# Kernel optimization log

Measured on AMD Instinct MI355X. Metric: run time of the kernel, lower is better.

Reference implementation:

```python
import jax, jax.numpy as jnp
import numpy as np

B, N, F_IN, F_OUT, H = 8, 1024, 128, 128, 8
D_K = F_OUT // H
NEG = -1.0e9


def setup_inputs() -> dict:
    key = jax.random.key(0)
    ks = jax.random.split(key, 10)
    X = jax.random.normal(ks[0], (B, N, F_IN), dtype=jnp.float32)
    A = (jax.random.uniform(ks[1], (B, N, N)) < 0.1).astype(jnp.float32)
    A = jnp.maximum(A, jnp.eye(N, dtype=jnp.float32)[None])
    s_in = 1.0 / np.sqrt(F_IN)
    s_out = 1.0 / np.sqrt(F_OUT)
    Wq = jax.random.uniform(ks[2], (F_OUT, F_IN), minval=-s_in, maxval=s_in)
    bq = jax.random.uniform(ks[3], (F_OUT,), minval=-s_in, maxval=s_in)
    Wk = jax.random.uniform(ks[4], (F_OUT, F_IN), minval=-s_in, maxval=s_in)
    bk = jax.random.uniform(ks[5], (F_OUT,), minval=-s_in, maxval=s_in)
    Wv = jax.random.uniform(ks[6], (F_OUT, F_IN), minval=-s_in, maxval=s_in)
    bv = jax.random.uniform(ks[7], (F_OUT,), minval=-s_in, maxval=s_in)
    Wo = jax.random.uniform(ks[8], (F_OUT, F_OUT), minval=-s_out, maxval=s_out)
    bo = jax.random.uniform(ks[9], (F_OUT,), minval=-s_out, maxval=s_out)
    return {"X": X, "A": A, "Wq": Wq, "bq": bq, "Wk": Wk, "bk": bk,
            "Wv": Wv, "bv": bv, "Wo": Wo, "bo": bo}


def reference(X, A, Wq, bq, Wk, bk, Wv, bv, Wo, bo):
    # QKV projections (nn.Linear: x @ W.T + b), split into heads
    Q = (X @ Wq.T + bq).reshape(B, N, H, D_K).transpose(0, 2, 1, 3)  # [B,H,N,d]
    K = (X @ Wk.T + bk).reshape(B, N, H, D_K).transpose(0, 2, 1, 3)
    V = (X @ Wv.T + bv).reshape(B, N, H, D_K).transpose(0, 2, 1, 3)
    scores = jnp.einsum('bhnd,bhmd->bhnm', Q, K) / jnp.sqrt(
        jnp.asarray(D_K, dtype=Q.dtype))
    # adjacency mask: entries with A<=0 set to -1e9 (matches masked_fill)
    scores = jnp.where(A[:, None, :, :] > 0, scores, NEG)
    attn = jax.nn.softmax(scores, axis=-1)  # dropout is identity at eval
    out = jnp.einsum('bhnm,bhmd->bhnd', attn, V)
    out = out.transpose(0, 2, 1, 3).reshape(B, N, H * D_K)
    return out @ Wo.T + bo
```

## Files before the change

kernel.cpp:

```cpp
#include <hip/hip_runtime.h>
#include <hip/hip_bf16.h>


#define BATCH 8
#define NNODE 1024
#define FEAT  128
#define NHEAD 8
#define CHUNKW 96
#define SPADW  100

typedef __attribute__((ext_vector_type(8))) short short8v;
typedef __attribute__((ext_vector_type(4))) float float4v;

__device__ __forceinline__ unsigned short f2bf(float f) {
  union { float f; unsigned u; } c; c.f = f;
  unsigned u = c.u;
  u += 0x7fff + ((u >> 16) & 1);
  return (unsigned short)(u >> 16);
}
__device__ __forceinline__ float bf2f(unsigned short h) {
  union { unsigned u; float f; } c; c.u = ((unsigned)h) << 16;
  return c.f;
}


__global__ __launch_bounds__(256) void wconv_kernel(
    const float* __restrict__ Wq, const float* __restrict__ Wk,
    const float* __restrict__ Wv, const float* __restrict__ Wo,
    unsigned short* __restrict__ Wh, unsigned short* __restrict__ Wl) {
  const int m = blockIdx.x >> 3;
  const int p = blockIdx.x & 7;
  const float* src = (m == 0) ? Wq : (m == 1) ? Wk : (m == 2) ? Wv : Wo;
  const int c = p * 16 + (threadIdx.x >> 4);
  const int k0 = (threadIdx.x & 15) * 8;
  const float4 a = *(const float4*)&src[c * 128 + k0];
  const float4 b = *(const float4*)&src[c * 128 + k0 + 4];
  const float xs[8] = {a.x, a.y, a.z, a.w, b.x, b.y, b.z, b.w};
  short8v h8, l8;
  #pragma unroll
  for (int e = 0; e < 8; ++e) {
    const unsigned short hs = f2bf(xs[e]);
    h8[e] = (short)hs;
    l8[e] = (short)f2bf(xs[e] - bf2f(hs));
  }
  const int ks = k0 >> 5;
  const int kg = (k0 >> 3) & 3;
  const int lanep = (c & 15) + 16 * kg;
  const size_t off = ((((size_t)m * 8 + p) * 4 + ks) * 64 + lanep) * 8;
  *(short8v*)&Wh[off] = h8;
  *(short8v*)&Wl[off] = l8;
}

__global__ __launch_bounds__(256) void pack_x_kernel(
    const float* __restrict__ X,
    unsigned short* __restrict__ Xh, unsigned short* __restrict__ Xl) {
  const int rb = blockIdx.x;
  const int ks = threadIdx.x >> 6;
  const int lane = threadIdx.x & 63;
  const int r = rb * 16 + (lane & 15);
  const int k0 = ks * 32 + (lane >> 4) * 8;
  const float4 a = *(const float4*)&X[(size_t)r * 128 + k0];
  const float4 b = *(const float4*)&X[(size_t)r * 128 + k0 + 4];
  const float xs[8] = {a.x, a.y, a.z, a.w, b.x, b.y, b.z, b.w};
  short8v h8, l8;
  #pragma unroll
  for (int e = 0; e < 8; ++e) {
    const unsigned short hs = f2bf(xs[e]);
    h8[e] = (short)hs;
    l8[e] = (short)f2bf(xs[e] - bf2f(hs));
  }
  const size_t off = (((size_t)rb * 4 + ks) * 64 + lane) * 8;
  *(short8v*)&Xh[off] = h8;
  *(short8v*)&Xl[off] = l8;
}

__device__ __forceinline__ void mfma_body(
    const unsigned short* __restrict__ Wh, const unsigned short* __restrict__ Wl,
    int wtile0, const short8v* aH, const short8v* aL, float4v* acc) {
  const int l = threadIdx.x & 63;
  #pragma unroll
  for (int ks = 0; ks < 4; ++ks) {
    #pragma unroll
    for (int nt = 0; nt < 4; ++nt) {
      const size_t wb = ((((size_t)wtile0 + nt) * 4 + ks) * 64 + l) * 8;
      const short8v bh = *(const short8v*)&Wh[wb];
      const short8v bl = *(const short8v*)&Wl[wb];
      acc[nt] = __builtin_amdgcn_mfma_f32_16x16x32_bf16(aL[ks], bh, acc[nt], 0, 0, 0);
      acc[nt] = __builtin_amdgcn_mfma_f32_16x16x32_bf16(aH[ks], bl, acc[nt], 0, 0, 0);
      acc[nt] = __builtin_amdgcn_mfma_f32_16x16x32_bf16(aH[ks], bh, acc[nt], 0, 0, 0);
    }
  }
}

__global__ __launch_bounds__(256) void qkv_mfma_kernel(
    const unsigned short* __restrict__ Xh, const unsigned short* __restrict__ Xl,
    const unsigned short* __restrict__ Wh, const unsigned short* __restrict__ Wl,
    const float* __restrict__ bq, const float* __restrict__ bk,
    const float* __restrict__ bv,
    unsigned short* __restrict__ Q, unsigned short* __restrict__ K,
    unsigned short* __restrict__ V) {
  const int w = threadIdx.x >> 6;
  const int l = threadIdx.x & 63;
  const int rb = blockIdx.x * 4 + w;
  const int c0 = blockIdx.y * 64;
  const int m = blockIdx.z;
  const float* bias = (m == 0) ? bq : (m == 1) ? bk : bv;
  unsigned short* dst = (m == 0) ? Q : (m == 1) ? K : V;
  const float scale = (m == 0) ? 0.25f : 1.0f;

  short8v aH[4], aL[4];
  #pragma unroll
  for (int ks = 0; ks < 4; ++ks) {
    const size_t ab = (((size_t)rb * 4 + ks) * 64 + l) * 8;
    aH[ks] = *(const short8v*)&Xh[ab];
    aL[ks] = *(const short8v*)&Xl[ab];
  }
  float4v acc[4] = {};
  mfma_body(Wh, Wl, m * 8 + blockIdx.y * 4, aH, aL, acc);

  const int row16 = l & 15;
  const int kgrp = l >> 4;
  #pragma unroll
  for (int nt = 0; nt < 4; ++nt) {
    const int col = c0 + nt * 16 + row16;
    const float bcol = bias[col];
    #pragma unroll
    for (int r = 0; r < 4; ++r) {
      const int row = rb * 16 + kgrp * 4 + r;
      dst[(size_t)row * 128 + col] = f2bf((acc[nt][r] + bcol) * scale);
    }
  }
}

__global__ __launch_bounds__(256) void out_mfma_kernel(
    const unsigned short* __restrict__ Yh, const unsigned short* __restrict__ Yl,
    const unsigned short* __restrict__ Wh, const unsigned short* __restrict__ Wl,
    const float* __restrict__ bias, float* __restrict__ out) {
  const int w = threadIdx.x >> 6;
  const int l = threadIdx.x & 63;
  const int rb = blockIdx.x * 4 + w;
  const int c0 = blockIdx.y * 64;

  short8v aH[4], aL[4];
  #pragma unroll
  for (int ks = 0; ks < 4; ++ks) {
    const size_t ab = (((size_t)rb * 4 + ks) * 64 + l) * 8;
    aH[ks] = *(const short8v*)&Yh[ab];
    aL[ks] = *(const short8v*)&Yl[ab];
  }
  float4v acc[4] = {};
  mfma_body(Wh, Wl, 3 * 8 + blockIdx.y * 4, aH, aL, acc);

  const int row16 = l & 15;
  const int kgrp = l >> 4;
  #pragma unroll
  for (int nt = 0; nt < 4; ++nt) {
    const int col = c0 + nt * 16 + row16;
    const float bcol = bias[col];
    #pragma unroll
    for (int r = 0; r < 4; ++r) {
      const int row = rb * 16 + kgrp * 4 + r;
      out[(size_t)row * 128 + col] = acc[nt][r] + bcol;
    }
  }
}

__global__ __launch_bounds__(256) void attn_kernel(
    const unsigned short* __restrict__ Qb, const unsigned short* __restrict__ Kb,
    const unsigned short* __restrict__ Vb, const float* __restrict__ A,
    unsigned short* __restrict__ Yh, unsigned short* __restrict__ Yl) {
  __shared__ float sS[4][NHEAD][SPADW];
  __shared__ unsigned short sIdx[4][512];
  __shared__ float sAx[2][2][64];
  __shared__ float sAy[2][2][64];
  __shared__ float sLh[2][2][NHEAD];

  const int t = threadIdx.x;
  const int w = t >> 6;
  const int lane = t & 63;
  const int pw = w >> 1;
  const int half = w & 1;
  const int b = blockIdx.x & 7;
  const int i = ((blockIdx.x >> 3) << 1) + pw;
  const size_t bBase = (size_t)b * NNODE;
  const size_t rowQ = (bBase + i) * FEAT;

  float q0, q1, q2, q3;
  {
    const ushort4 qu = *(const ushort4*)&Qb[rowQ + 4 * (lane & 31)];
    q0 = bf2f(qu.x); q1 = bf2f(qu.y); q2 = bf2f(qu.z); q3 = bf2f(qu.w);
  }

  const float* Arow = A + (bBase + i) * NNODE + half * 512;
  const unsigned long long lt = (1ull << lane) - 1ull;
  int cnt = 0;
  #pragma unroll
  for (int r = 0; r < 2; ++r) {
    const float4 av = *(const float4*)&Arow[r * 256 + lane * 4];
    const unsigned long long m0 = __ballot(av.x > 0.f);
    const unsigned long long m1 = __ballot(av.y > 0.f);
    const unsigned long long m2 = __ballot(av.z > 0.f);
    const unsigned long long m3 = __ballot(av.w > 0.f);
    const int c0n = __popcll(m0), c1n = __popcll(m1), c2n = __popcll(m2);
    const int j0 = half * 512 + r * 256 + lane * 4;
    if (av.x > 0.f) sIdx[w][cnt + __popcll(m0 & lt)] = (unsigned short)j0;
    if (av.y > 0.f) sIdx[w][cnt + c0n + __popcll(m1 & lt)] = (unsigned short)(j0 + 1);
    if (av.z > 0.f) sIdx[w][cnt + c0n + c1n + __popcll(m2 & lt)] = (unsigned short)(j0 + 2);
    if (av.w > 0.f) sIdx[w][cnt + c0n + c1n + c2n + __popcll(m3 & lt)] = (unsigned short)(j0 + 3);
    cnt += c0n + c1n + c2n + __popcll(m3);
  }

  const int side = lane >> 5;
  const int sgrp = (lane & 31) >> 2;
  const int h = lane >> 3;
  float lacc = 0.f;
  float ax = 0.f, ay = 0.f;

  for (int c0 = 0; c0 < cnt; c0 += CHUNKW) {
    const int cs = min(cnt - c0, CHUNKW);

    for (int p2 = 0; p2 < cs; p2 += 2) {
      const int s = p2 + side;
      const bool valid = s < cs;
      const int j = sIdx[w][valid ? (c0 + s) : c0];
      const ushort4 ku = *(const ushort4*)&Kb[(bBase + j) * FEAT + 4 * (lane & 31)];
      float part = q0 * bf2f(ku.x) + q1 * bf2f(ku.y) +
                   q2 * bf2f(ku.z) + q3 * bf2f(ku.w);
      part += __shfl_xor(part, 1);
      part += __shfl_xor(part, 2);
      if (valid && (lane & 3) == 0) {
        const float p = __expf(part - 8.0f);
        sS[w][sgrp][s] = p;
        lacc += p;
      }
    }

    #pragma unroll 8
    for (int s = 0; s < cs; ++s) {
      const int j = sIdx[w][c0 + s];
      const unsigned vu = *(const unsigned*)&Vb[(bBase + j) * FEAT + 2 * lane];
      const float p = sS[w][h][s];
      ax += p * bf2f((unsigned short)(vu & 0xffff));
      ay += p * bf2f((unsigned short)(vu >> 16));
    }
  }

  const float lhv = __shfl(lacc, 4 * (lane & 7)) +
                    __shfl(lacc, 32 + 4 * (lane & 7));

  sAx[pw][half][lane] = ax;
  sAy[pw][half][lane] = ay;
  if (lane < NHEAD) sLh[pw][half][lane] = lhv;
  __syncthreads();

  const float axT = sAx[pw][0][lane] + sAx[pw][1][lane];
  const float ayT = sAy[pw][0][lane] + sAy[pw][1][lane];
  const float lT = sLh[pw][0][h] + sLh[pw][1][h];
  const float y0 = axT / lT;
  const float y1 = ayT / lT;

  const int grow = (int)(bBase + i);
  const int rb = grow >> 4;
  const int row16 = grow & 15;
  const int f0 = 2 * lane;
  const int ks = f0 >> 5;
  const int kg = (f0 >> 3) & 3;
  const int e0 = f0 & 7;
  const size_t off = (((size_t)rb * 4 + ks) * 64 + row16 + 16 * kg) * 8 + e0;
  const unsigned short h0 = f2bf(y0), h1 = f2bf(y1);
  if (half == 0) {
    *(unsigned*)&Yh[off] = (unsigned)h0 | ((unsigned)h1 << 16);
  } else {
    const unsigned short l0 = f2bf(y0 - bf2f(h0));
    const unsigned short l1 = f2bf(y1 - bf2f(h1));
    *(unsigned*)&Yl[off] = (unsigned)l0 | ((unsigned)l1 << 16);
  }
}

extern "C" void kernel_launch(void* const* d_in, const int* in_sizes, int n_in,
                              void* d_out, int out_size, void* d_ws, size_t ws_size,
                              hipStream_t stream) {
  const float* X  = (const float*)d_in[0];
  const float* A  = (const float*)d_in[1];
  const float* Wq = (const float*)d_in[2];
  const float* bq = (const float*)d_in[3];
  const float* Wk = (const float*)d_in[4];
  const float* bk = (const float*)d_in[5];
  const float* Wv = (const float*)d_in[6];
  const float* bv = (const float*)d_in[7];
  const float* Wo = (const float*)d_in[8];
  const float* bo = (const float*)d_in[9];
  float* out = (float*)d_out;

  const size_t mat = (size_t)BATCH * NNODE * FEAT;
  unsigned short* Q  = (unsigned short*)d_ws;
  unsigned short* K  = Q + mat;
  unsigned short* V  = K + mat;
  unsigned short* Yh = V + mat;
  unsigned short* Yl = Yh + mat;
  unsigned short* Xh = Yl + mat;
  unsigned short* Xl = Xh + mat;
  unsigned short* Wh = Xl + mat;
  unsigned short* Wl = Wh + 4 * 16384;

  hipLaunchKernelGGL(wconv_kernel, dim3(32), dim3(256), 0, stream,
                     Wq, Wk, Wv, Wo, Wh, Wl);
  hipLaunchKernelGGL(pack_x_kernel, dim3(512), dim3(256), 0, stream, X, Xh, Xl);
  hipLaunchKernelGGL(qkv_mfma_kernel, dim3(128, 2, 3), dim3(256), 0, stream,
                     Xh, Xl, Wh, Wl, bq, bk, bv, Q, K, V);
  hipLaunchKernelGGL(attn_kernel, dim3(4096), dim3(256), 0, stream,
                     Q, K, V, A, Yh, Yl);
  hipLaunchKernelGGL(out_mfma_kernel, dim3(128, 2), dim3(256), 0, stream,
                     Yh, Yl, Wh, Wl, bo, out);
}
```

Before: 146.8 us.

## Fuse all five stages into one cooperative persistent kernel with grid syncs

Replaces the five separate launches (weight conversion, X packing, QKV GEMM, attention, output GEMM) with a single cooperative kernel of 512 blocks. The blocks step through the stages and separate them with grid.sync(), looping over the attention tasks. The aim is to remove per-launch overhead and inter-kernel gaps. In exchange, occupancy is capped at 512 resident blocks, attention tasks are serialised in 8 iterations per block, and grid-wide barriers plus a cooperative-launch path add their own cost.

```diff
diff --git a/kernel.cpp b/kernel.cpp
--- a/kernel.cpp
+++ b/kernel.cpp
@@ -1,5 +1,8 @@
 #include <hip/hip_runtime.h>
 #include <hip/hip_bf16.h>
+#include <hip/hip_cooperative_groups.h>
+
+namespace cg = cooperative_groups;
 
 
 #define BATCH 8
@@ -24,12 +27,12 @@
 }
 
 
-__global__ __launch_bounds__(256) void wconv_kernel(
-    const float* __restrict__ Wq, const float* __restrict__ Wk,
+__device__ __forceinline__ void do_wconv(
+    int wb, const float* __restrict__ Wq, const float* __restrict__ Wk,
     const float* __restrict__ Wv, const float* __restrict__ Wo,
     unsigned short* __restrict__ Wh, unsigned short* __restrict__ Wl) {
-  const int m = blockIdx.x >> 3;
-  const int p = blockIdx.x & 7;
+  const int m = wb >> 3;
+  const int p = wb & 7;
   const float* src = (m == 0) ? Wq : (m == 1) ? Wk : (m == 2) ? Wv : Wo;
   const int c = p * 16 + (threadIdx.x >> 4);
   const int k0 = (threadIdx.x & 15) * 8;
@@ -51,10 +54,9 @@
   *(short8v*)&Wl[off] = l8;
 }
 
-__global__ __launch_bounds__(256) void pack_x_kernel(
-    const float* __restrict__ X,
+__device__ __forceinline__ void do_pack_x(
+    int rb, const float* __restrict__ X,
     unsigned short* __restrict__ Xh, unsigned short* __restrict__ Xl) {
-  const int rb = blockIdx.x;
   const int ks = threadIdx.x >> 6;
   const int lane = threadIdx.x & 63;
   const int r = rb * 16 + (lane & 15);
@@ -92,7 +94,8 @@
   }
 }
 
-__global__ __launch_bounds__(256) void qkv_mfma_kernel(
+__device__ __forceinline__ void do_qkv(
+    int tx, int ty, int tz,
     const unsigned short* __restrict__ Xh, const unsigned short* __restrict__ Xl,
     const unsigned short* __restrict__ Wh, const unsigned short* __restrict__ Wl,
     const float* __restrict__ bq, const float* __restrict__ bk,
@@ -101,12 +104,11 @@
     unsigned short* __restrict__ V) {
   const int w = threadIdx.x >> 6;
   const int l = threadIdx.x & 63;
-  const int rb = blockIdx.x * 4 + w;
-  const int c0 = blockIdx.y * 64;
-  const int m = blockIdx.z;
-  const float* bias = (m == 0) ? bq : (m == 1) ? bk : bv;
-  unsigned short* dst = (m == 0) ? Q : (m == 1) ? K : V;
-  const float scale = (m == 0) ? 0.25f : 1.0f;
+  const int rb = tx * 4 + w;
+  const int c0 = ty * 64;
+  const float* bias = (tz == 0) ? bq : (tz == 1) ? bk : bv;
+  unsigned short* dst = (tz == 0) ? Q : (tz == 1) ? K : V;
+  const float scale = (tz == 0) ? 0.25f : 1.0f;
 
   short8v aH[4], aL[4];
   #pragma unroll
@@ -116,7 +118,7 @@
     aL[ks] = *(const short8v*)&Xl[ab];
   }
   float4v acc[4] = {};
-  mfma_body(Wh, Wl, m * 8 + blockIdx.y * 4, aH, aL, acc);
+  mfma_body(Wh, Wl, tz * 8 + ty * 4, aH, aL, acc);
 
   const int row16 = l & 15;
   const int kgrp = l >> 4;
@@ -132,14 +134,15 @@
   }
 }
 
-__global__ __launch_bounds__(256) void out_mfma_kernel(
+__device__ __forceinline__ void do_out(
+    int tx, int ty,
     const unsigned short* __restrict__ Yh, const unsigned short* __restrict__ Yl,
     const unsigned short* __restrict__ Wh, const unsigned short* __restrict__ Wl,
     const float* __restrict__ bias, float* __restrict__ out) {
   const int w = threadIdx.x >> 6;
   const int l = threadIdx.x & 63;
-  const int rb = blockIdx.x * 4 + w;
-  const int c0 = blockIdx.y * 64;
+  const int rb = tx * 4 + w;
+  const int c0 = ty * 64;
 
   short8v aH[4], aL[4];
   #pragma unroll
@@ -149,7 +152,7 @@
     aL[ks] = *(const short8v*)&Yl[ab];
   }
   float4v acc[4] = {};
-  mfma_body(Wh, Wl, 3 * 8 + blockIdx.y * 4, aH, aL, acc);
+  mfma_body(Wh, Wl, 3 * 8 + ty * 4, aH, aL, acc);
 
   const int row16 = l & 15;
   const int kgrp = l >> 4;
@@ -165,7 +168,8 @@
   }
 }
 
-__global__ __launch_bounds__(256) void attn_kernel(
+__device__ __forceinline__ void do_attn(
+    int task,
     const unsigned short* __restrict__ Qb, const unsigned short* __restrict__ Kb,
     const unsigned short* __restrict__ Vb, const float* __restrict__ A,
     unsigned short* __restrict__ Yh, unsigned short* __restrict__ Yl) {
@@ -175,13 +179,15 @@
   __shared__ float sAy[2][2][64];
   __shared__ float sLh[2][2][NHEAD];
 
+  __syncthreads();
+
   const int t = threadIdx.x;
   const int w = t >> 6;
   const int lane = t & 63;
   const int pw = w >> 1;
   const int half = w & 1;
-  const int b = blockIdx.x & 7;
-  const int i = ((blockIdx.x >> 3) << 1) + pw;
+  const int b = task & 7;
+  const int i = ((task >> 3) << 1) + pw;
   const size_t bBase = (size_t)b * NNODE;
   const size_t rowQ = (bBase + i) * FEAT;
 
@@ -277,6 +283,41 @@
   }
 }
 
+__global__ __launch_bounds__(256, 2) void fused_kernel(
+    const float* __restrict__ X, const float* __restrict__ A,
+    const float* __restrict__ Wq, const float* __restrict__ bq,
+    const float* __restrict__ Wk, const float* __restrict__ bk,
+    const float* __restrict__ Wv, const float* __restrict__ bv,
+    const float* __restrict__ Wo, const float* __restrict__ bo,
+    float* __restrict__ out,
+    unsigned short* __restrict__ Qd, unsigned short* __restrict__ Kd,
+    unsigned short* __restrict__ Vd,
+    unsigned short* __restrict__ Yh, unsigned short* __restrict__ Yl,
+    unsigned short* __restrict__ Xh, unsigned short* __restrict__ Xl,
+    unsigned short* __restrict__ Wh, unsigned short* __restrict__ Wl) {
+  cg::grid_group grid = cg::this_grid();
+  const int bid = blockIdx.x;
+
+  do_pack_x(bid, X, Xh, Xl);
+  if (bid < 32) do_wconv(bid, Wq, Wk, Wv, Wo, Wh, Wl);
+  grid.sync();
+
+  do_qkv(bid & 127, (bid >> 7) & 1, bid >> 8, Xh, Xl, Wh, Wl,
+         bq, bk, bv, Qd, Kd, Vd);
+  if (bid < 256) {
+    const int t1 = bid + 512;
+    do_qkv(t1 & 127, (t1 >> 7) & 1, t1 >> 8, Xh, Xl, Wh, Wl,
+           bq, bk, bv, Qd, Kd, Vd);
+  }
+  grid.sync();
+
+  for (int it = 0; it < 8; ++it)
+    do_attn(bid + 512 * it, Qd, Kd, Vd, A, Yh, Yl);
+  grid.sync();
+
+  if (bid < 256) do_out(bid & 127, bid >> 7, Yh, Yl, Wh, Wl, bo, out);
+}
+
 extern "C" void kernel_launch(void* const* d_in, const int* in_sizes, int n_in,
                               void* d_out, int out_size, void* d_ws, size_t ws_size,
                               hipStream_t stream) {
@@ -293,23 +334,18 @@
   float* out = (float*)d_out;
 
   const size_t mat = (size_t)BATCH * NNODE * FEAT;
-  unsigned short* Q  = (unsigned short*)d_ws;
-  unsigned short* K  = Q + mat;
-  unsigned short* V  = K + mat;
-  unsigned short* Yh = V + mat;
+  unsigned short* Qd = (unsigned short*)d_ws;
+  unsigned short* Kd = Qd + mat;
+  unsigned short* Vd = Kd + mat;
+  unsigned short* Yh = Vd + mat;
   unsigned short* Yl = Yh + mat;
   unsigned short* Xh = Yl + mat;
   unsigned short* Xl = Xh + mat;
   unsigned short* Wh = Xl + mat;
   unsigned short* Wl = Wh + 4 * 16384;
 
-  hipLaunchKernelGGL(wconv_kernel, dim3(32), dim3(256), 0, stream,
-                     Wq, Wk, Wv, Wo, Wh, Wl);
-  hipLaunchKernelGGL(pack_x_kernel, dim3(512), dim3(256), 0, stream, X, Xh, Xl);
-  hipLaunchKernelGGL(qkv_mfma_kernel, dim3(128, 2, 3), dim3(256), 0, stream,
-                     Xh, Xl, Wh, Wl, bq, bk, bv, Q, K, V);
-  hipLaunchKernelGGL(attn_kernel, dim3(4096), dim3(256), 0, stream,
-                     Q, K, V, A, Yh, Yl);
-  hipLaunchKernelGGL(out_mfma_kernel, dim3(128, 2), dim3(256), 0, stream,
-                     Yh, Yl, Wh, Wl, bo, out);
-}
+  void* args[] = {&X, &A, &Wq, &bq, &Wk, &bk, &Wv, &bv, &Wo, &bo,
+                  &out, &Qd, &Kd, &Vd, &Yh, &Yl, &Xh, &Xl, &Wh, &Wl};
+  hipLaunchCooperativeKernel((const void*)fused_kernel, dim3(512), dim3(256),
+                             args, 0, stream);
+}
```

Result: slower. 405.0 us (+176.0%).

## Fuse output projection into attention kernel and merge prep kernels

Applied to the files above, without the earlier changes.

Merges the weight and X packing kernels into one launch and fuses the output projection into the attention kernel as an fp32 FMA loop reading Wo directly. This removes the Yh/Yl split-bf16 round trip and a separate MFMA launch. The QKV GEMM is also split into narrower column tiles to raise block count. In exchange, each attention block reads the full 64KB Wo from cache and does a scalar 2x128x128 GEMV per block, which adds ALU and L2 traffic to an already heavy kernel.

```diff
diff --git a/kernel.cpp b/kernel.cpp
--- a/kernel.cpp
+++ b/kernel.cpp
@@ -24,71 +24,55 @@
 }
 
 
-__global__ __launch_bounds__(256) void wconv_kernel(
+__global__ __launch_bounds__(256) void prep_kernel(
+    const float* __restrict__ X,
     const float* __restrict__ Wq, const float* __restrict__ Wk,
-    const float* __restrict__ Wv, const float* __restrict__ Wo,
+    const float* __restrict__ Wv,
+    unsigned short* __restrict__ Xh, unsigned short* __restrict__ Xl,
     unsigned short* __restrict__ Wh, unsigned short* __restrict__ Wl) {
-  const int m = blockIdx.x >> 3;
-  const int p = blockIdx.x & 7;
-  const float* src = (m == 0) ? Wq : (m == 1) ? Wk : (m == 2) ? Wv : Wo;
-  const int c = p * 16 + (threadIdx.x >> 4);
-  const int k0 = (threadIdx.x & 15) * 8;
-  const float4 a = *(const float4*)&src[c * 128 + k0];
-  const float4 b = *(const float4*)&src[c * 128 + k0 + 4];
-  const float xs[8] = {a.x, a.y, a.z, a.w, b.x, b.y, b.z, b.w};
-  short8v h8, l8;
-  #pragma unroll
-  for (int e = 0; e < 8; ++e) {
-    const unsigned short hs = f2bf(xs[e]);
-    h8[e] = (short)hs;
-    l8[e] = (short)f2bf(xs[e] - bf2f(hs));
-  }
-  const int ks = k0 >> 5;
-  const int kg = (k0 >> 3) & 3;
-  const int lanep = (c & 15) + 16 * kg;
-  const size_t off = ((((size_t)m * 8 + p) * 4 + ks) * 64 + lanep) * 8;
-  *(short8v*)&Wh[off] = h8;
-  *(short8v*)&Wl[off] = l8;
-}
-
-__global__ __launch_bounds__(256) void pack_x_kernel(
-    const float* __restrict__ X,
-    unsigned short* __restrict__ Xh, unsigned short* __restrict__ Xl) {
-  const int rb = blockIdx.x;
-  const int ks = threadIdx.x >> 6;
-  const int lane = threadIdx.x & 63;
-  const int r = rb * 16 + (lane & 15);
-  const int k0 = ks * 32 + (lane >> 4) * 8;
-  const float4 a = *(const float4*)&X[(size_t)r * 128 + k0];
-  const float4 b = *(const float4*)&X[(size_t)r * 128 + k0 + 4];
-  const float xs[8] = {a.x, a.y, a.z, a.w, b.x, b.y, b.z, b.w};
-  short8v h8, l8;
-  #pragma unroll
-  for (int e = 0; e < 8; ++e) {
-    const unsigned short hs = f2bf(xs[e]);
-    h8[e] = (short)hs;
-    l8[e] = (short)f2bf(xs[e] - bf2f(hs));
-  }
-  const size_t off = (((size_t)rb * 4 + ks) * 64 + lane) * 8;
-  *(short8v*)&Xh[off] = h8;
-  *(short8v*)&Xl[off] = l8;
-}
-
-__device__ __forceinline__ void mfma_body(
-    const unsigned short* __restrict__ Wh, const unsigned short* __restrict__ Wl,
-    int wtile0, const short8v* aH, const short8v* aL, float4v* acc) {
-  const int l = threadIdx.x & 63;
-  #pragma unroll
-  for (int ks = 0; ks < 4; ++ks) {
-    #pragma unroll
-    for (int nt = 0; nt < 4; ++nt) {
-      const size_t wb = ((((size_t)wtile0 + nt) * 4 + ks) * 64 + l) * 8;
-      const short8v bh = *(const short8v*)&Wh[wb];
-      const short8v bl = *(const short8v*)&Wl[wb];
-      acc[nt] = __builtin_amdgcn_mfma_f32_16x16x32_bf16(aL[ks], bh, acc[nt], 0, 0, 0);
-      acc[nt] = __builtin_amdgcn_mfma_f32_16x16x32_bf16(aH[ks], bl, acc[nt], 0, 0, 0);
-      acc[nt] = __builtin_amdgcn_mfma_f32_16x16x32_bf16(aH[ks], bh, acc[nt], 0, 0, 0);
-    }
+  const int bid = blockIdx.x;
+  if (bid < 512) {
+    const int rb = bid;
+    const int ks = threadIdx.x >> 6;
+    const int lane = threadIdx.x & 63;
+    const int r = rb * 16 + (lane & 15);
+    const int k0 = ks * 32 + (lane >> 4) * 8;
+    const float4 a = *(const float4*)&X[(size_t)r * 128 + k0];
+    const float4 b = *(const float4*)&X[(size_t)r * 128 + k0 + 4];
+    const float xs[8] = {a.x, a.y, a.z, a.w, b.x, b.y, b.z, b.w};
+    short8v h8, l8;
+    #pragma unroll
+    for (int e = 0; e < 8; ++e) {
+      const unsigned short hs = f2bf(xs[e]);
+      h8[e] = (short)hs;
+      l8[e] = (short)f2bf(xs[e] - bf2f(hs));
+    }
+    const size_t off = (((size_t)rb * 4 + ks) * 64 + lane) * 8;
+    *(short8v*)&Xh[off] = h8;
+    *(short8v*)&Xl[off] = l8;
+  } else {
+    const int wb = bid - 512;
+    const int m = wb >> 3;
+    const int p = wb & 7;
+    const float* src = (m == 0) ? Wq : (m == 1) ? Wk : Wv;
+    const int c = p * 16 + (threadIdx.x >> 4);
+    const int k0 = (threadIdx.x & 15) * 8;
+    const float4 a = *(const float4*)&src[c * 128 + k0];
+    const float4 b = *(const float4*)&src[c * 128 + k0 + 4];
+    const float xs[8] = {a.x, a.y, a.z, a.w, b.x, b.y, b.z, b.w};
+    short8v h8, l8;
+    #pragma unroll
+    for (int e = 0; e < 8; ++e) {
+      const unsigned short hs = f2bf(xs[e]);
+      h8[e] = (short)hs;
+      l8[e] = (short)f2bf(xs[e] - bf2f(hs));
+    }
+    const int ks = k0 >> 5;
+    const int kg = (k0 >> 3) & 3;
+    const int lanep = (c & 15) + 16 * kg;
+    const size_t off = ((((size_t)m * 8 + p) * 4 + ks) * 64 + lanep) * 8;
+    *(short8v*)&Wh[off] = h8;
+    *(short8v*)&Wl[off] = l8;
   }
 }
 
@@ -102,11 +86,12 @@
   const int w = threadIdx.x >> 6;
   const int l = threadIdx.x & 63;
   const int rb = blockIdx.x * 4 + w;
-  const int c0 = blockIdx.y * 64;
-  const int m = blockIdx.z;
-  const float* bias = (m == 0) ? bq : (m == 1) ? bk : bv;
-  unsigned short* dst = (m == 0) ? Q : (m == 1) ? K : V;
-  const float scale = (m == 0) ? 0.25f : 1.0f;
+  const int ty = blockIdx.y;
+  const int tz = blockIdx.z;
+  const int c0 = ty * 32;
+  const float* bias = (tz == 0) ? bq : (tz == 1) ? bk : bv;
+  unsigned short* dst = (tz == 0) ? Q : (tz == 1) ? K : V;
+  const float scale = (tz == 0) ? 0.25f : 1.0f;
 
   short8v aH[4], aL[4];
   #pragma unroll
@@ -115,13 +100,25 @@
     aH[ks] = *(const short8v*)&Xh[ab];
     aL[ks] = *(const short8v*)&Xl[ab];
   }
-  float4v acc[4] = {};
-  mfma_body(Wh, Wl, m * 8 + blockIdx.y * 4, aH, aL, acc);
+  float4v acc[2] = {};
+  const int wtile0 = tz * 8 + ty * 2;
+  #pragma unroll
+  for (int ks = 0; ks < 4; ++ks) {
+    #pragma unroll
+    for (int nt = 0; nt < 2; ++nt) {
+      const size_t wb = ((((size_t)wtile0 + nt) * 4 + ks) * 64 + l) * 8;
+      const short8v bh = *(const short8v*)&Wh[wb];
+      const short8v bl = *(const short8v*)&Wl[wb];
+      acc[nt] = __builtin_amdgcn_mfma_f32_16x16x32_bf16(aL[ks], bh, acc[nt], 0, 0, 0);
+      acc[nt] = __builtin_amdgcn_mfma_f32_16x16x32_bf16(aH[ks], bl, acc[nt], 0, 0, 0);
+      acc[nt] = __builtin_amdgcn_mfma_f32_16x16x32_bf16(aH[ks], bh, acc[nt], 0, 0, 0);
+    }
+  }
 
   const int row16 = l & 15;
   const int kgrp = l >> 4;
   #pragma unroll
-  for (int nt = 0; nt < 4; ++nt) {
+  for (int nt = 0; nt < 2; ++nt) {
     const int col = c0 + nt * 16 + row16;
     const float bcol = bias[col];
     #pragma unroll
@@ -132,48 +129,17 @@
   }
 }
 
-__global__ __launch_bounds__(256) void out_mfma_kernel(
-    const unsigned short* __restrict__ Yh, const unsigned short* __restrict__ Yl,
-    const unsigned short* __restrict__ Wh, const unsigned short* __restrict__ Wl,
-    const float* __restrict__ bias, float* __restrict__ out) {
-  const int w = threadIdx.x >> 6;
-  const int l = threadIdx.x & 63;
-  const int rb = blockIdx.x * 4 + w;
-  const int c0 = blockIdx.y * 64;
-
-  short8v aH[4], aL[4];
-  #pragma unroll
-  for (int ks = 0; ks < 4; ++ks) {
-    const size_t ab = (((size_t)rb * 4 + ks) * 64 + l) * 8;
-    aH[ks] = *(const short8v*)&Yh[ab];
-    aL[ks] = *(const short8v*)&Yl[ab];
-  }
-  float4v acc[4] = {};
-  mfma_body(Wh, Wl, 3 * 8 + blockIdx.y * 4, aH, aL, acc);
-
-  const int row16 = l & 15;
-  const int kgrp = l >> 4;
-  #pragma unroll
-  for (int nt = 0; nt < 4; ++nt) {
-    const int col = c0 + nt * 16 + row16;
-    const float bcol = bias[col];
-    #pragma unroll
-    for (int r = 0; r < 4; ++r) {
-      const int row = rb * 16 + kgrp * 4 + r;
-      out[(size_t)row * 128 + col] = acc[nt][r] + bcol;
-    }
-  }
-}
-
-__global__ __launch_bounds__(256) void attn_kernel(
+__global__ __launch_bounds__(256) void attn_out_kernel(
     const unsigned short* __restrict__ Qb, const unsigned short* __restrict__ Kb,
     const unsigned short* __restrict__ Vb, const float* __restrict__ A,
-    unsigned short* __restrict__ Yh, unsigned short* __restrict__ Yl) {
+    const float* __restrict__ Wo, const float* __restrict__ bo,
+    float* __restrict__ out) {
   __shared__ float sS[4][NHEAD][SPADW];
   __shared__ unsigned short sIdx[4][512];
   __shared__ float sAx[2][2][64];
   __shared__ float sAy[2][2][64];
   __shared__ float sLh[2][2][NHEAD];
+  __shared__ float sY[2][FEAT];
 
   const int t = threadIdx.x;
   const int w = t >> 6;
@@ -181,7 +147,8 @@
   const int pw = w >> 1;
   const int half = w & 1;
   const int b = blockIdx.x & 7;
-  const int i = ((blockIdx.x >> 3) << 1) + pw;
+  const int i0 = ((blockIdx.x >> 3) << 1);
+  const int i = i0 + pw;
   const size_t bBase = (size_t)b * NNODE;
   const size_t rowQ = (bBase + i) * FEAT;
 
@@ -253,28 +220,26 @@
   if (lane < NHEAD) sLh[pw][half][lane] = lhv;
   __syncthreads();
 
-  const float axT = sAx[pw][0][lane] + sAx[pw][1][lane];
-  const float ayT = sAy[pw][0][lane] + sAy[pw][1][lane];
-  const float lT = sLh[pw][0][h] + sLh[pw][1][h];
-  const float y0 = axT / lT;
-  const float y1 = ayT / lT;
-
-  const int grow = (int)(bBase + i);
-  const int rb = grow >> 4;
-  const int row16 = grow & 15;
-  const int f0 = 2 * lane;
-  const int ks = f0 >> 5;
-  const int kg = (f0 >> 3) & 3;
-  const int e0 = f0 & 7;
-  const size_t off = (((size_t)rb * 4 + ks) * 64 + row16 + 16 * kg) * 8 + e0;
-  const unsigned short h0 = f2bf(y0), h1 = f2bf(y1);
   if (half == 0) {
-    *(unsigned*)&Yh[off] = (unsigned)h0 | ((unsigned)h1 << 16);
-  } else {
-    const unsigned short l0 = f2bf(y0 - bf2f(h0));
-    const unsigned short l1 = f2bf(y1 - bf2f(h1));
-    *(unsigned*)&Yl[off] = (unsigned)l0 | ((unsigned)l1 << 16);
-  }
+    const float axT = sAx[pw][0][lane] + sAx[pw][1][lane];
+    const float ayT = sAy[pw][0][lane] + sAy[pw][1][lane];
+    const float lT = sLh[pw][0][h] + sLh[pw][1][h];
+    sY[pw][2 * lane] = axT / lT;
+    sY[pw][2 * lane + 1] = ayT / lT;
+  }
+  __syncthreads();
+
+  const int row = t >> 7;
+  const int c = t & 127;
+  const float* WoR = Wo + (size_t)c * FEAT;
+  const float* Yr = sY[row];
+  float acc = bo[c];
+  #pragma unroll 8
+  for (int k = 0; k < FEAT; k += 4) {
+    const float4 wv = *(const float4*)&WoR[k];
+    acc += Yr[k] * wv.x + Yr[k + 1] * wv.y + Yr[k + 2] * wv.z + Yr[k + 3] * wv.w;
+  }
+  out[(bBase + i0 + row) * FEAT + c] = acc;
 }
 
 extern "C" void kernel_launch(void* const* d_in, const int* in_sizes, int n_in,
@@ -293,23 +258,18 @@
   float* out = (float*)d_out;
 
   const size_t mat = (size_t)BATCH * NNODE * FEAT;
-  unsigned short* Q  = (unsigned short*)d_ws;
-  unsigned short* K  = Q + mat;
-  unsigned short* V  = K + mat;
-  unsigned short* Yh = V + mat;
-  unsigned short* Yl = Yh + mat;
-  unsigned short* Xh = Yl + mat;
+  unsigned short* Qd = (unsigned short*)d_ws;
+  unsigned short* Kd = Qd + mat;
+  unsigned short* Vd = Kd + mat;
+  unsigned short* Xh = Vd + mat;
   unsigned short* Xl = Xh + mat;
   unsigned short* Wh = Xl + mat;
-  unsigned short* Wl = Wh + 4 * 16384;
-
-  hipLaunchKernelGGL(wconv_kernel, dim3(32), dim3(256), 0, stream,
-                     Wq, Wk, Wv, Wo, Wh, Wl);
-  hipLaunchKernelGGL(pack_x_kernel, dim3(512), dim3(256), 0, stream, X, Xh, Xl);
-  hipLaunchKernelGGL(qkv_mfma_kernel, dim3(128, 2, 3), dim3(256), 0, stream,
-                     Xh, Xl, Wh, Wl, bq, bk, bv, Q, K, V);
-  hipLaunchKernelGGL(attn_kernel, dim3(4096), dim3(256), 0, stream,
-                     Q, K, V, A, Yh, Yl);
-  hipLaunchKernelGGL(out_mfma_kernel, dim3(128, 2), dim3(256), 0, stream,
-                     Yh, Yl, Wh, Wl, bo, out);
-}
+  unsigned short* Wl = Wh + 3 * 16384;
+
+  hipLaunchKernelGGL(prep_kernel, dim3(536), dim3(256), 0, stream,
+                     X, Wq, Wk, Wv, Xh, Xl, Wh, Wl);
+  hipLaunchKernelGGL(qkv_mfma_kernel, dim3(128, 4, 3), dim3(256), 0, stream,
+                     Xh, Xl, Wh, Wl, bq, bk, bv, Qd, Kd, Vd);
+  hipLaunchKernelGGL(attn_out_kernel, dim3(4096), dim3(256), 0, stream,
+                     Qd, Kd, Vd, A, Wo, bo, out);
+}
```

After: 190.1 us. 29.5% more time.
